# Optimization experiments

Hardware: AMD Instinct MI355X
Metric: run time of the kernel (lower is better)

## Reference

```python
import jax, jax.numpy as jnp
import numpy as np

B, L, D, H = 2, 2048, 1024, 16
HD = D // H
NEG = -1000000000.0


def setup_inputs() -> dict:
    key = jax.random.key(0)
    ks = jax.random.split(key, 11)
    s = 1.0 / np.sqrt(D)
    return {
        "q": jax.random.normal(ks[0], (B, L, D), jnp.float32),
        "k": jax.random.normal(ks[1], (B, L, D), jnp.float32),
        "v": jax.random.normal(ks[2], (B, L, D), jnp.float32),
        "mask": jnp.ones((B, L, L), jnp.int32),
        "Wq": jax.random.normal(ks[3], (D, D), jnp.float32) * s,
        "bq": jnp.zeros((D,), jnp.float32),
        "Wk": jax.random.normal(ks[4], (D, D), jnp.float32) * s,
        "bk": jnp.zeros((D,), jnp.float32),
        "Wv": jax.random.normal(ks[5], (D, D), jnp.float32) * s,
        "bv": jnp.zeros((D,), jnp.float32),
        "Wo": jax.random.normal(ks[6], (D, D), jnp.float32) * s,
        "bo": jnp.zeros((D,), jnp.float32),
    }


def _split(x):
    # [B,L,D] -> [B,H,L,HD]
    return x.reshape(B, L, H, HD).transpose(0, 2, 1, 3)


def reference(q, k, v, mask, Wq, bq, Wk, bk, Wv, bv, Wo, bo):
    Q = _split(q @ Wq.T + bq)
    K = _split(k @ Wk.T + bk)
    V = _split(v @ Wv.T + bv)
    scores = jnp.einsum("bhqd,bhkd->bhqk", Q, K) / jnp.sqrt(jnp.float32(HD))
    m = mask[:, None, :, :]  # [B,1,L,L]
    scores = jnp.where(m == 0, NEG, scores)
    attn = jax.nn.softmax(scores, axis=-1)
    out = jnp.einsum("bhqk,bhkd->bhqd", attn, V)
    out = out.transpose(0, 2, 1, 3).reshape(B, L, D)
    out = out @ Wo.T + bo
    return out, attn
```

## Files before the change

### kernel.cpp

```cpp
#include <hip/hip_runtime.h>
#include <stdint.h>

#define BSZ 2
#define LSEQ 2048
#define DMOD 1024
#define NH 16
#define HDSZ 64
#define NT (LSEQ / 128)

typedef __attribute__((ext_vector_type(8))) short short8;
typedef __attribute__((ext_vector_type(4))) float f32x4;
typedef __attribute__((ext_vector_type(4))) unsigned short u16x4;
typedef __attribute__((ext_vector_type(4))) int i32x4;

#define MFMA16(a, b, c) __builtin_amdgcn_mfma_f32_16x16x32_bf16((a), (b), (c), 0, 0, 0)
#define EXP2F(x) __builtin_amdgcn_exp2f(x)

__device__ __forceinline__ unsigned short f2bf(float f) {
  union { float f; unsigned u; } x; x.f = f;
  unsigned u = x.u + 0x7fffu + ((x.u >> 16) & 1u);
  return (unsigned short)(u >> 16);
}

__device__ __forceinline__ unsigned cvt_pk_bf16(float lo, float hi) {
  unsigned r;
  asm("v_cvt_pk_bf16_f32 %0, %1, %2" : "=v"(r) : "v"(lo), "v"(hi));
  return r;
}

__device__ __forceinline__ short8 pack8_pk(f32x4 lo, f32x4 hi) {
  union { short8 s; unsigned u[4]; } r;
  r.u[0] = cvt_pk_bf16(lo[0], lo[1]);
  r.u[1] = cvt_pk_bf16(lo[2], lo[3]);
  r.u[2] = cvt_pk_bf16(hi[0], hi[1]);
  r.u[3] = cvt_pk_bf16(hi[2], hi[3]);
  return r.s;
}

__device__ __forceinline__ u16x4 pack4_pk(float a, float b, float c, float d) {
  union { u16x4 p; unsigned u[2]; } r;
  r.u[0] = cvt_pk_bf16(a, b);
  r.u[1] = cvt_pk_bf16(c, d);
  return r.p;
}

template <int AF32, int OUTF32>
__global__ __launch_bounds__(256) void gemm_bt(
    const void* __restrict__ A0, const void* __restrict__ A1, const void* __restrict__ A2,
    const float* __restrict__ W0, const float* __restrict__ W1, const float* __restrict__ W2,
    const float* __restrict__ b0, const float* __restrict__ b1, const float* __restrict__ b2,
    void* __restrict__ C0, void* __restrict__ C1, void* __restrict__ C2,
    float s0, float s1, float s2, int vtz, int M, int N, int K,
    const int* __restrict__ mask, int* __restrict__ flags) {
  const int z = blockIdx.z;
  const int tid = threadIdx.x;
  __shared__ int red[4];

  if (z == 3) {
    const int t0 = (blockIdx.x + 32 * blockIdx.y) * 2;
#pragma unroll
    for (int t = t0; t < t0 + 2; ++t) {
      const int b_ = t >> 8, qt = (t >> 4) & 15, ktt = t & 15;
      const int r = tid >> 1, c = (tid & 1) * 64;
      const int* mr = mask + (size_t)b_ * LSEQ * LSEQ + (size_t)(qt * 128 + r) * LSEQ +
                      ktt * 128 + c;
      int ok = 1;
#pragma unroll
      for (int j = 0; j < 16; j++) {
        i32x4 v = __builtin_nontemporal_load((const i32x4*)(mr + j * 4));
        ok &= (v[0] != 0) & (v[1] != 0) & (v[2] != 0) & (v[3] != 0);
      }
      unsigned long long vote = __ballot(ok);
      if ((tid & 63) == 0) red[tid >> 6] = (vote == ~0ull) ? 1 : 0;
      __syncthreads();
      if (tid == 0) flags[(b_ * 16 + qt) * 16 + ktt] = red[0] & red[1] & red[2] & red[3];
      __syncthreads();
    }
    return;
  }

  const void* A = (z == 0) ? A0 : ((z == 1) ? A1 : A2);
  const float* W = (z == 0) ? W0 : ((z == 1) ? W1 : W2);
  const float* bias = (z == 0) ? b0 : ((z == 1) ? b1 : b2);
  void* Cout = (z == 0) ? C0 : ((z == 1) ? C1 : C2);
  const float scale = (z == 0) ? s0 : ((z == 1) ? s1 : s2);

  __shared__ unsigned short As[128 * 40];
  __shared__ unsigned short Bs[128 * 40];

  const int lane = tid & 63;
  const int wid = tid >> 6;
  const int bm = blockIdx.x, bn = blockIdx.y;
  const int wm = (wid >> 1) * 64, wn = (wid & 1) * 64;

  f32x4 acc[4][4];
#pragma unroll
  for (int i = 0; i < 4; i++)
#pragma unroll
    for (int j = 0; j < 4; j++) acc[i][j] = (f32x4){0.f, 0.f, 0.f, 0.f};

  const int r0 = tid >> 2;
  const int c0 = (tid & 3) * 8;
  const float* Wg = W + (size_t)(bn * 128 + r0) * K + c0;

  f32x4 vaf[2][2], vbf[2][2];
  short8 vah[2];
  if constexpr (AF32) {
    const float* Ag = (const float*)A + (size_t)(bm * 128 + r0) * K + c0;
#pragma unroll
    for (int j = 0; j < 2; j++) {
      vaf[j][0] = *(const f32x4*)(Ag + (size_t)(j * 64) * K);
      vaf[j][1] = *(const f32x4*)(Ag + (size_t)(j * 64) * K + 4);
    }
  } else {
    const unsigned short* Ag = (const unsigned short*)A + (size_t)(bm * 128 + r0) * K + c0;
#pragma unroll
    for (int j = 0; j < 2; j++) vah[j] = *(const short8*)(Ag + (size_t)(j * 64) * K);
  }
#pragma unroll
  for (int j = 0; j < 2; j++) {
    vbf[j][0] = *(const f32x4*)(Wg + (size_t)(j * 64) * K);
    vbf[j][1] = *(const f32x4*)(Wg + (size_t)(j * 64) * K + 4);
  }

  for (int k0 = 0; k0 < K; k0 += 32) {
#pragma unroll
    for (int j = 0; j < 2; j++) {
      if constexpr (AF32)
        *(short8*)&As[(j * 64 + r0) * 40 + c0] = pack8_pk(vaf[j][0], vaf[j][1]);
      else
        *(short8*)&As[(j * 64 + r0) * 40 + c0] = vah[j];
      *(short8*)&Bs[(j * 64 + r0) * 40 + c0] = pack8_pk(vbf[j][0], vbf[j][1]);
    }
    __syncthreads();
    if (k0 + 32 < K) {
      if constexpr (AF32) {
        const float* Ag = (const float*)A + (size_t)(bm * 128 + r0) * K + c0 + k0 + 32;
#pragma unroll
        for (int j = 0; j < 2; j++) {
          vaf[j][0] = *(const f32x4*)(Ag + (size_t)(j * 64) * K);
          vaf[j][1] = *(const f32x4*)(Ag + (size_t)(j * 64) * K + 4);
        }
      } else {
        const unsigned short* Ag =
            (const unsigned short*)A + (size_t)(bm * 128 + r0) * K + c0 + k0 + 32;
#pragma unroll
        for (int j = 0; j < 2; j++) vah[j] = *(const short8*)(Ag + (size_t)(j * 64) * K);
      }
#pragma unroll
      for (int j = 0; j < 2; j++) {
        vbf[j][0] = *(const f32x4*)(Wg + (size_t)(j * 64) * K + k0 + 32);
        vbf[j][1] = *(const f32x4*)(Wg + (size_t)(j * 64) * K + k0 + 36);
      }
    }
    short8 af[4], bf[4];
#pragma unroll
    for (int i = 0; i < 4; i++)
      af[i] = *(const short8*)&As[(wm + i * 16 + (lane & 15)) * 40 + (lane >> 4) * 8];
#pragma unroll
    for (int i = 0; i < 4; i++)
      bf[i] = *(const short8*)&Bs[(wn + i * 16 + (lane & 15)) * 40 + (lane >> 4) * 8];
#pragma unroll
    for (int i = 0; i < 4; i++)
#pragma unroll
      for (int j = 0; j < 4; j++) acc[i][j] = MFMA16(af[i], bf[j], acc[i][j]);
    __syncthreads();
  }

  const bool vtrans = (z == vtz);
  const int crow = bm * 128 + wm + ((lane >> 4) & 3) * 4;
#pragma unroll
  for (int j = 0; j < 4; j++) {
    const int col = bn * 128 + wn + j * 16 + (lane & 15);
    const float bv = bias[col];
#pragma unroll
    for (int i = 0; i < 4; i++) {
      if (OUTF32) {
#pragma unroll
        for (int r = 0; r < 4; r++) {
          float vvv = (acc[i][j][r] + bv) * scale;
          ((float*)Cout)[(size_t)(crow + i * 16 + r) * N + col] = vvv;
        }
      } else if (vtrans) {
        u16x4 pk = pack4_pk((acc[i][j][0] + bv) * scale, (acc[i][j][1] + bv) * scale,
                            (acc[i][j][2] + bv) * scale, (acc[i][j][3] + bv) * scale);
        const int row = crow + i * 16;
        unsigned short* dst = (unsigned short*)Cout +
                              (size_t)(row >> 11) * DMOD * LSEQ + (size_t)col * LSEQ +
                              (row & (LSEQ - 1));
        *(u16x4*)dst = pk;
      } else {
#pragma unroll
        for (int r = 0; r < 4; r++) {
          float vvv = (acc[i][j][r] + bv) * scale;
          ((unsigned short*)Cout)[(size_t)(crow + i * 16 + r) * N + col] =
              (unsigned short)(cvt_pk_bf16(vvv, vvv) & 0xffffu);
        }
      }
    }
  }
}

__global__ __launch_bounds__(256) void attn_kernel(
    const unsigned short* __restrict__ Qp, const unsigned short* __restrict__ Kp,
    const unsigned short* __restrict__ Vt, const int* __restrict__ mask,
    const int* __restrict__ flags, float* __restrict__ attn_out,
    unsigned short* __restrict__ ctx) {
  __shared__ unsigned short Ks[128 * 64];
  __shared__ unsigned short Ps[4][32][136];

  const int tid = threadIdx.x, lane = tid & 63, wid = tid >> 6;
  const int l15 = lane & 15, lg = lane >> 4;

  const int wgid = blockIdx.x + gridDim.x * blockIdx.y;
  const int jj = wgid >> 3;
  const int bh = (wgid & 7) * 4 + (jj >> 4);
  const int qt = jj & 15;
  const int q0 = qt * 128;
  const int b = bh >> 4, h = bh & 15;

  const unsigned short* Qh = Qp + (size_t)b * LSEQ * DMOD + h * HDSZ;
  const unsigned short* Kh = Kp + (size_t)b * LSEQ * DMOD + h * HDSZ;
  const unsigned short* Vh = Vt + (size_t)b * DMOD * LSEQ + (size_t)h * HDSZ * LSEQ;
  const int* mb = mask + (size_t)b * LSEQ * LSEQ;
  const int* frow = flags + (b * 16 + qt) * 16;
  float* ah = attn_out + (size_t)bh * LSEQ * LSEQ;

  const int wq0 = q0 + wid * 32;

  short8 qf[2][2];
#pragma unroll
  for (int fq = 0; fq < 2; fq++)
#pragma unroll
    for (int ks = 0; ks < 2; ks++)
      qf[fq][ks] = *(const short8*)(Qh + (size_t)(wq0 + fq * 16 + l15) * DMOD +
                                    ks * 32 + lg * 8);

  const int sr = tid >> 1;
  const unsigned short* Kst = Kh + (size_t)sr * DMOD + (tid & 1) * 32;
  const int swz_w = (sr & 7) << 4;

  float den[2] = {0.f, 0.f};
  short8 ka[4];
#pragma unroll
  for (int j = 0; j < 4; j++) ka[j] = *(const short8*)(Kst + j * 8);

  for (int kt = 0; kt < NT; ++kt) {
    __syncthreads();
#pragma unroll
    for (int j = 0; j < 4; j++)
      *(short8*)&Ks[sr * 64 + (((((tid & 1) * 64) + j * 16) ^ swz_w) >> 1)] = ka[j];
    __syncthreads();
    if (kt + 1 < NT) {
#pragma unroll
      for (int j = 0; j < 4; j++)
        ka[j] = *(const short8*)(Kst + (size_t)(kt + 1) * 128 * DMOD + j * 8);
    }
    const bool fast = frow[kt] != 0;
    if (fast) {
#pragma unroll
      for (int fn = 0; fn < 8; fn++) {
        const int krow = fn * 16 + l15;
        const int rb = krow * 64, rx = (krow & 7) << 4;
        short8 kf0 = *(const short8*)&Ks[rb + (((lg * 16) ^ rx) >> 1)];
        short8 kf1 = *(const short8*)&Ks[rb + (((64 + lg * 16) ^ rx) >> 1)];
#pragma unroll
        for (int fq = 0; fq < 2; fq++) {
          f32x4 s = (f32x4){0.f, 0.f, 0.f, 0.f};
          s = MFMA16(kf0, qf[fq][0], s);
          s = MFMA16(kf1, qf[fq][1], s);
          den[fq] += EXP2F(s[0]) + EXP2F(s[1]) + EXP2F(s[2]) + EXP2F(s[3]);
        }
      }
    } else {
      const int k0 = kt * 128;
#pragma unroll
      for (int fn = 0; fn < 8; fn++) {
        const int krow = fn * 16 + l15;
        const int rb = krow * 64, rx = (krow & 7) << 4;
        short8 kf0 = *(const short8*)&Ks[rb + (((lg * 16) ^ rx) >> 1)];
        short8 kf1 = *(const short8*)&Ks[rb + (((64 + lg * 16) ^ rx) >> 1)];
#pragma unroll
        for (int fq = 0; fq < 2; fq++) {
          const int qrow = wq0 + fq * 16 + l15;
          f32x4 s = (f32x4){0.f, 0.f, 0.f, 0.f};
          s = MFMA16(kf0, qf[fq][0], s);
          s = MFMA16(kf1, qf[fq][1], s);
          i32x4 m4 = *(const i32x4*)(mb + (size_t)qrow * LSEQ + k0 + fn * 16 + lg * 4);
          den[fq] += (m4[0] != 0) ? EXP2F(s[0]) : 0.f;
          den[fq] += (m4[1] != 0) ? EXP2F(s[1]) : 0.f;
          den[fq] += (m4[2] != 0) ? EXP2F(s[2]) : 0.f;
          den[fq] += (m4[3] != 0) ? EXP2F(s[3]) : 0.f;
        }
      }
    }
  }
  float inv[2];
#pragma unroll
  for (int fq = 0; fq < 2; fq++) {
    den[fq] += __shfl_xor(den[fq], 16);
    den[fq] += __shfl_xor(den[fq], 32);
    inv[fq] = 1.0f / den[fq];
  }

  f32x4 oacc[2][4];
#pragma unroll
  for (int fq = 0; fq < 2; fq++)
#pragma unroll
    for (int fd = 0; fd < 4; fd++) oacc[fq][fd] = (f32x4){0.f, 0.f, 0.f, 0.f};

#pragma unroll
  for (int j = 0; j < 4; j++) ka[j] = *(const short8*)(Kst + j * 8);

  const unsigned short* Vbase = Vh + (size_t)l15 * LSEQ + lg * 8;

  for (int kt = 0; kt < NT; ++kt) {
    const int k0 = kt * 128;
    __syncthreads();
#pragma unroll
    for (int j = 0; j < 4; j++)
      *(short8*)&Ks[sr * 64 + (((((tid & 1) * 64) + j * 16) ^ swz_w) >> 1)] = ka[j];
    __syncthreads();
    if (kt + 1 < NT) {
#pragma unroll
      for (int j = 0; j < 4; j++)
        ka[j] = *(const short8*)(Kst + (size_t)(kt + 1) * 128 * DMOD + j * 8);
    }
    short8 vf[4][4];
#pragma unroll
    for (int fd = 0; fd < 4; fd++)
#pragma unroll
      for (int ks = 0; ks < 4; ks++)
        vf[fd][ks] = *(const short8*)(Vbase + (size_t)(fd * 16) * LSEQ + k0 + ks * 32);

    const bool fast = frow[kt] != 0;
    if (fast) {
#pragma unroll
      for (int fn = 0; fn < 8; fn++) {
        const int krow = fn * 16 + l15;
        const int rb = krow * 64, rx = (krow & 7) << 4;
        short8 kf0 = *(const short8*)&Ks[rb + (((lg * 16) ^ rx) >> 1)];
        short8 kf1 = *(const short8*)&Ks[rb + (((64 + lg * 16) ^ rx) >> 1)];
#pragma unroll
        for (int fq = 0; fq < 2; fq++) {
          f32x4 s = (f32x4){0.f, 0.f, 0.f, 0.f};
          s = MFMA16(kf0, qf[fq][0], s);
          s = MFMA16(kf1, qf[fq][1], s);
          f32x4 a;
          a[0] = EXP2F(s[0]) * inv[fq];
          a[1] = EXP2F(s[1]) * inv[fq];
          a[2] = EXP2F(s[2]) * inv[fq];
          a[3] = EXP2F(s[3]) * inv[fq];
          union { u16x4 pk; unsigned u[2]; } P;
          P.u[0] = cvt_pk_bf16(a[0], a[1]);
          P.u[1] = cvt_pk_bf16(a[2], a[3]);
          *(u16x4*)&Ps[wid][fq * 16 + l15][fn * 16 + lg * 4] = P.pk;
        }
      }
    } else {
#pragma unroll
      for (int fn = 0; fn < 8; fn++) {
        const int krow = fn * 16 + l15;
        const int rb = krow * 64, rx = (krow & 7) << 4;
        short8 kf0 = *(const short8*)&Ks[rb + (((lg * 16) ^ rx) >> 1)];
        short8 kf1 = *(const short8*)&Ks[rb + (((64 + lg * 16) ^ rx) >> 1)];
#pragma unroll
        for (int fq = 0; fq < 2; fq++) {
          const int qrow = wq0 + fq * 16 + l15;
          f32x4 s = (f32x4){0.f, 0.f, 0.f, 0.f};
          s = MFMA16(kf0, qf[fq][0], s);
          s = MFMA16(kf1, qf[fq][1], s);
          i32x4 m4 = *(const i32x4*)(mb + (size_t)qrow * LSEQ + k0 + fn * 16 + lg * 4);
          f32x4 a;
          a[0] = (m4[0] != 0) ? EXP2F(s[0]) * inv[fq] : 0.f;
          a[1] = (m4[1] != 0) ? EXP2F(s[1]) * inv[fq] : 0.f;
          a[2] = (m4[2] != 0) ? EXP2F(s[2]) * inv[fq] : 0.f;
          a[3] = (m4[3] != 0) ? EXP2F(s[3]) * inv[fq] : 0.f;
          union { u16x4 pk; unsigned u[2]; } P;
          P.u[0] = cvt_pk_bf16(a[0], a[1]);
          P.u[1] = cvt_pk_bf16(a[2], a[3]);
          *(u16x4*)&Ps[wid][fq * 16 + l15][fn * 16 + lg * 4] = P.pk;
        }
      }
    }
    short8 pa2[2][4];
#pragma unroll
    for (int fq = 0; fq < 2; fq++)
#pragma unroll
      for (int ks = 0; ks < 4; ks++)
        pa2[fq][ks] = *(const short8*)&Ps[wid][fq * 16 + l15][ks * 32 + lg * 8];
#pragma unroll
    for (int fd = 0; fd < 4; fd++)
#pragma unroll
      for (int fq = 0; fq < 2; fq++)
#pragma unroll
        for (int ks = 0; ks < 4; ks++)
          oacc[fq][fd] = MFMA16(pa2[fq][ks], vf[fd][ks], oacc[fq][fd]);

    {
      float* abase = ah + (size_t)wq0 * LSEQ + k0;
      const int rsel = lane >> 5, csel = (lane & 31) * 4;
#pragma unroll
      for (int i = 0; i < 16; i++) {
        const int qoff = i * 2 + rsel;
        unsigned long long d = *(const unsigned long long*)&Ps[wid][qoff][csel];
        unsigned d0 = (unsigned)d, d1 = (unsigned)(d >> 32);
        union { unsigned u; float f; } t0, t1, t2, t3;
        t0.u = d0 << 16;
        t1.u = d0 & 0xffff0000u;
        t2.u = d1 << 16;
        t3.u = d1 & 0xffff0000u;
        f32x4 a = (f32x4){t0.f, t1.f, t2.f, t3.f};
        __builtin_nontemporal_store(a, (f32x4*)(abase + (size_t)qoff * LSEQ + csel));
      }
    }
  }

  unsigned short* ch = ctx + (size_t)b * LSEQ * DMOD + h * HDSZ;
#pragma unroll
  for (int fq = 0; fq < 2; fq++)
#pragma unroll
    for (int fd = 0; fd < 4; fd++) {
      u16x4 pk = pack4_pk(oacc[fq][fd][0], oacc[fq][fd][1], oacc[fq][fd][2],
                          oacc[fq][fd][3]);
#pragma unroll
      for (int r = 0; r < 4; r++) {
        const int qr = wq0 + fq * 16 + lg * 4 + r;
        ch[(size_t)qr * DMOD + fd * 16 + l15] = pk[r];
      }
    }
}

extern "C" void kernel_launch(void* const* d_in, const int* in_sizes, int n_in,
                              void* d_out, int out_size, void* d_ws, size_t ws_size,
                              hipStream_t stream) {
  const float* q = (const float*)d_in[0];
  const float* k = (const float*)d_in[1];
  const float* v = (const float*)d_in[2];
  const int* mask = (const int*)d_in[3];
  const float* Wq = (const float*)d_in[4];
  const float* bq = (const float*)d_in[5];
  const float* Wk = (const float*)d_in[6];
  const float* bk = (const float*)d_in[7];
  const float* Wv = (const float*)d_in[8];
  const float* bv = (const float*)d_in[9];
  const float* Wo = (const float*)d_in[10];
  const float* bo = (const float*)d_in[11];

  float* out = (float*)d_out;
  float* attn = out + (size_t)BSZ * LSEQ * DMOD;

  const size_t NQKV = (size_t)BSZ * LSEQ * DMOD;

  int* flags = (int*)out;

  unsigned short* Qp = (unsigned short*)d_ws;
  unsigned short* Kp = Qp + NQKV;
  unsigned short* Vt = Kp + NQKV;
  unsigned short* ctx = Vt + NQKV;

  gemm_bt<1, 0><<<dim3(32, 8, 4), 256, 0, stream>>>(
      q, k, v, Wq, Wk, Wv, bq, bk, bv, (void*)Qp, (void*)Kp, (void*)Vt,
      0.18033688011112042f, 1.0f, 1.0f, 2, BSZ * LSEQ, DMOD, DMOD, mask, flags);

  attn_kernel<<<dim3(LSEQ / 128, BSZ * NH), 256, 0, stream>>>(Qp, Kp, Vt, mask, flags,
                                                              attn, ctx);

  gemm_bt<0, 1><<<dim3(32, 8, 1), 256, 0, stream>>>(
      ctx, ctx, ctx, Wo, Wo, Wo, bo, bo, bo, (void*)out, (void*)out, (void*)out,
      1.0f, 1.0f, 1.0f, -1, BSZ * LSEQ, DMOD, DMOD, nullptr, nullptr);
}
```

Before: 229.3 us.

## Halve attention query tile to 64 rows per block, doubling grid size

Each attention workgroup now handles 64 query rows (16 per wave) instead of 128, so the grid grows from 512 to 1024 blocks and per-thread register use drops (single Q fragment, 4 output accumulators, smaller P buffer in LDS). V fragments are loaded per output column group just before use instead of all up front. This aims to raise occupancy and spread the bandwidth-heavy attention-probability writes over more CUs, at the cost of each K tile being loaded and QK^T recomputed by twice as many blocks.

```diff
diff --git a/kernel.cpp b/kernel.cpp
--- a/kernel.cpp
+++ b/kernel.cpp
@@ -207,40 +207,38 @@
     const int* __restrict__ flags, float* __restrict__ attn_out,
     unsigned short* __restrict__ ctx) {
   __shared__ unsigned short Ks[128 * 64];
-  __shared__ unsigned short Ps[4][32][136];
+  __shared__ unsigned short Ps[4][16][136];
 
   const int tid = threadIdx.x, lane = tid & 63, wid = tid >> 6;
   const int l15 = lane & 15, lg = lane >> 4;
 
   const int wgid = blockIdx.x + gridDim.x * blockIdx.y;
   const int jj = wgid >> 3;
-  const int bh = (wgid & 7) * 4 + (jj >> 4);
-  const int qt = jj & 15;
-  const int q0 = qt * 128;
+  const int bh = (wgid & 7) * 4 + (jj >> 5);
+  const int qt = jj & 31;
+  const int q0 = qt * 64;
   const int b = bh >> 4, h = bh & 15;
 
   const unsigned short* Qh = Qp + (size_t)b * LSEQ * DMOD + h * HDSZ;
   const unsigned short* Kh = Kp + (size_t)b * LSEQ * DMOD + h * HDSZ;
   const unsigned short* Vh = Vt + (size_t)b * DMOD * LSEQ + (size_t)h * HDSZ * LSEQ;
   const int* mb = mask + (size_t)b * LSEQ * LSEQ;
-  const int* frow = flags + (b * 16 + qt) * 16;
+  const int* frow = flags + (b * 16 + (q0 >> 7)) * 16;
   float* ah = attn_out + (size_t)bh * LSEQ * LSEQ;
 
-  const int wq0 = q0 + wid * 32;
-
-  short8 qf[2][2];
-#pragma unroll
-  for (int fq = 0; fq < 2; fq++)
-#pragma unroll
-    for (int ks = 0; ks < 2; ks++)
-      qf[fq][ks] = *(const short8*)(Qh + (size_t)(wq0 + fq * 16 + l15) * DMOD +
-                                    ks * 32 + lg * 8);
+  const int wq0 = q0 + wid * 16;
+  const int qrow = wq0 + l15;
+
+  short8 qf[2];
+#pragma unroll
+  for (int ks = 0; ks < 2; ks++)
+    qf[ks] = *(const short8*)(Qh + (size_t)qrow * DMOD + ks * 32 + lg * 8);
 
   const int sr = tid >> 1;
   const unsigned short* Kst = Kh + (size_t)sr * DMOD + (tid & 1) * 32;
   const int swz_w = (sr & 7) << 4;
 
-  float den[2] = {0.f, 0.f};
+  float den = 0.f;
   short8 ka[4];
 #pragma unroll
   for (int j = 0; j < 4; j++) ka[j] = *(const short8*)(Kst + j * 8);
@@ -264,13 +262,10 @@
         const int rb = krow * 64, rx = (krow & 7) << 4;
         short8 kf0 = *(const short8*)&Ks[rb + (((lg * 16) ^ rx) >> 1)];
         short8 kf1 = *(const short8*)&Ks[rb + (((64 + lg * 16) ^ rx) >> 1)];
-#pragma unroll
-        for (int fq = 0; fq < 2; fq++) {
-          f32x4 s = (f32x4){0.f, 0.f, 0.f, 0.f};
-          s = MFMA16(kf0, qf[fq][0], s);
-          s = MFMA16(kf1, qf[fq][1], s);
-          den[fq] += EXP2F(s[0]) + EXP2F(s[1]) + EXP2F(s[2]) + EXP2F(s[3]);
-        }
+        f32x4 s = (f32x4){0.f, 0.f, 0.f, 0.f};
+        s = MFMA16(kf0, qf[0], s);
+        s = MFMA16(kf1, qf[1], s);
+        den += EXP2F(s[0]) + EXP2F(s[1]) + EXP2F(s[2]) + EXP2F(s[3]);
       }
     } else {
       const int k0 = kt * 128;
@@ -280,34 +275,24 @@
         const int rb = krow * 64, rx = (krow & 7) << 4;
         short8 kf0 = *(const short8*)&Ks[rb + (((lg * 16) ^ rx) >> 1)];
         short8 kf1 = *(const short8*)&Ks[rb + (((64 + lg * 16) ^ rx) >> 1)];
-#pragma unroll
-        for (int fq = 0; fq < 2; fq++) {
-          const int qrow = wq0 + fq * 16 + l15;
-          f32x4 s = (f32x4){0.f, 0.f, 0.f, 0.f};
-          s = MFMA16(kf0, qf[fq][0], s);
-          s = MFMA16(kf1, qf[fq][1], s);
-          i32x4 m4 = *(const i32x4*)(mb + (size_t)qrow * LSEQ + k0 + fn * 16 + lg * 4);
-          den[fq] += (m4[0] != 0) ? EXP2F(s[0]) : 0.f;
-          den[fq] += (m4[1] != 0) ? EXP2F(s[1]) : 0.f;
-          den[fq] += (m4[2] != 0) ? EXP2F(s[2]) : 0.f;
-          den[fq] += (m4[3] != 0) ? EXP2F(s[3]) : 0.f;
-        }
-      }
-    }
-  }
-  float inv[2];
-#pragma unroll
-  for (int fq = 0; fq < 2; fq++) {
-    den[fq] += __shfl_xor(den[fq], 16);
-    den[fq] += __shfl_xor(den[fq], 32);
-    inv[fq] = 1.0f / den[fq];
-  }
-
-  f32x4 oacc[2][4];
-#pragma unroll
-  for (int fq = 0; fq < 2; fq++)
-#pragma unroll
-    for (int fd = 0; fd < 4; fd++) oacc[fq][fd] = (f32x4){0.f, 0.f, 0.f, 0.f};
+        f32x4 s = (f32x4){0.f, 0.f, 0.f, 0.f};
+        s = MFMA16(kf0, qf[0], s);
+        s = MFMA16(kf1, qf[1], s);
+        i32x4 m4 = *(const i32x4*)(mb + (size_t)qrow * LSEQ + k0 + fn * 16 + lg * 4);
+        den += (m4[0] != 0) ? EXP2F(s[0]) : 0.f;
+        den += (m4[1] != 0) ? EXP2F(s[1]) : 0.f;
+        den += (m4[2] != 0) ? EXP2F(s[2]) : 0.f;
+        den += (m4[3] != 0) ? EXP2F(s[3]) : 0.f;
+      }
+    }
+  }
+  den += __shfl_xor(den, 16);
+  den += __shfl_xor(den, 32);
+  const float inv = 1.0f / den;
+
+  f32x4 oacc[4];
+#pragma unroll
+  for (int fd = 0; fd < 4; fd++) oacc[fd] = (f32x4){0.f, 0.f, 0.f, 0.f};
 
 #pragma unroll
   for (int j = 0; j < 4; j++) ka[j] = *(const short8*)(Kst + j * 8);
@@ -326,12 +311,6 @@
       for (int j = 0; j < 4; j++)
         ka[j] = *(const short8*)(Kst + (size_t)(kt + 1) * 128 * DMOD + j * 8);
     }
-    short8 vf[4][4];
-#pragma unroll
-    for (int fd = 0; fd < 4; fd++)
-#pragma unroll
-      for (int ks = 0; ks < 4; ks++)
-        vf[fd][ks] = *(const short8*)(Vbase + (size_t)(fd * 16) * LSEQ + k0 + ks * 32);
 
     const bool fast = frow[kt] != 0;
     if (fast) {
@@ -341,21 +320,18 @@
         const int rb = krow * 64, rx = (krow & 7) << 4;
         short8 kf0 = *(const short8*)&Ks[rb + (((lg * 16) ^ rx) >> 1)];
         short8 kf1 = *(const short8*)&Ks[rb + (((64 + lg * 16) ^ rx) >> 1)];
-#pragma unroll
-        for (int fq = 0; fq < 2; fq++) {
-          f32x4 s = (f32x4){0.f, 0.f, 0.f, 0.f};
-          s = MFMA16(kf0, qf[fq][0], s);
-          s = MFMA16(kf1, qf[fq][1], s);
-          f32x4 a;
-          a[0] = EXP2F(s[0]) * inv[fq];
-          a[1] = EXP2F(s[1]) * inv[fq];
-          a[2] = EXP2F(s[2]) * inv[fq];
-          a[3] = EXP2F(s[3]) * inv[fq];
-          union { u16x4 pk; unsigned u[2]; } P;
-          P.u[0] = cvt_pk_bf16(a[0], a[1]);
-          P.u[1] = cvt_pk_bf16(a[2], a[3]);
-          *(u16x4*)&Ps[wid][fq * 16 + l15][fn * 16 + lg * 4] = P.pk;
-        }
+        f32x4 s = (f32x4){0.f, 0.f, 0.f, 0.f};
+        s = MFMA16(kf0, qf[0], s);
+        s = MFMA16(kf1, qf[1], s);
+        f32x4 a;
+        a[0] = EXP2F(s[0]) * inv;
+        a[1] = EXP2F(s[1]) * inv;
+        a[2] = EXP2F(s[2]) * inv;
+        a[3] = EXP2F(s[3]) * inv;
+        union { u16x4 pk; unsigned u[2]; } P;
+        P.u[0] = cvt_pk_bf16(a[0], a[1]);
+        P.u[1] = cvt_pk_bf16(a[2], a[3]);
+        *(u16x4*)&Ps[wid][l15][fn * 16 + lg * 4] = P.pk;
       }
     } else {
 #pragma unroll
@@ -364,44 +340,40 @@
         const int rb = krow * 64, rx = (krow & 7) << 4;
         short8 kf0 = *(const short8*)&Ks[rb + (((lg * 16) ^ rx) >> 1)];
         short8 kf1 = *(const short8*)&Ks[rb + (((64 + lg * 16) ^ rx) >> 1)];
-#pragma unroll
-        for (int fq = 0; fq < 2; fq++) {
-          const int qrow = wq0 + fq * 16 + l15;
-          f32x4 s = (f32x4){0.f, 0.f, 0.f, 0.f};
-          s = MFMA16(kf0, qf[fq][0], s);
-          s = MFMA16(kf1, qf[fq][1], s);
-          i32x4 m4 = *(const i32x4*)(mb + (size_t)qrow * LSEQ + k0 + fn * 16 + lg * 4);
-          f32x4 a;
-          a[0] = (m4[0] != 0) ? EXP2F(s[0]) * inv[fq] : 0.f;
-          a[1] = (m4[1] != 0) ? EXP2F(s[1]) * inv[fq] : 0.f;
-          a[2] = (m4[2] != 0) ? EXP2F(s[2]) * inv[fq] : 0.f;
-          a[3] = (m4[3] != 0) ? EXP2F(s[3]) * inv[fq] : 0.f;
-          union { u16x4 pk; unsigned u[2]; } P;
-          P.u[0] = cvt_pk_bf16(a[0], a[1]);
-          P.u[1] = cvt_pk_bf16(a[2], a[3]);
-          *(u16x4*)&Ps[wid][fq * 16 + l15][fn * 16 + lg * 4] = P.pk;
-        }
-      }
-    }
-    short8 pa2[2][4];
-#pragma unroll
-    for (int fq = 0; fq < 2; fq++)
+        f32x4 s = (f32x4){0.f, 0.f, 0.f, 0.f};
+        s = MFMA16(kf0, qf[0], s);
+        s = MFMA16(kf1, qf[1], s);
+        i32x4 m4 = *(const i32x4*)(mb + (size_t)qrow * LSEQ + k0 + fn * 16 + lg * 4);
+        f32x4 a;
+        a[0] = (m4[0] != 0) ? EXP2F(s[0]) * inv : 0.f;
+        a[1] = (m4[1] != 0) ? EXP2F(s[1]) * inv : 0.f;
+        a[2] = (m4[2] != 0) ? EXP2F(s[2]) * inv : 0.f;
+        a[3] = (m4[3] != 0) ? EXP2F(s[3]) * inv : 0.f;
+        union { u16x4 pk; unsigned u[2]; } P;
+        P.u[0] = cvt_pk_bf16(a[0], a[1]);
+        P.u[1] = cvt_pk_bf16(a[2], a[3]);
+        *(u16x4*)&Ps[wid][l15][fn * 16 + lg * 4] = P.pk;
+      }
+    }
+    short8 pa2[4];
+#pragma unroll
+    for (int ks = 0; ks < 4; ks++)
+      pa2[ks] = *(const short8*)&Ps[wid][l15][ks * 32 + lg * 8];
+#pragma unroll
+    for (int fd = 0; fd < 4; fd++) {
+      short8 vfd[4];
 #pragma unroll
       for (int ks = 0; ks < 4; ks++)
-        pa2[fq][ks] = *(const short8*)&Ps[wid][fq * 16 + l15][ks * 32 + lg * 8];
-#pragma unroll
-    for (int fd = 0; fd < 4; fd++)
-#pragma unroll
-      for (int fq = 0; fq < 2; fq++)
-#pragma unroll
-        for (int ks = 0; ks < 4; ks++)
-          oacc[fq][fd] = MFMA16(pa2[fq][ks], vf[fd][ks], oacc[fq][fd]);
+        vfd[ks] = *(const short8*)(Vbase + (size_t)(fd * 16) * LSEQ + k0 + ks * 32);
+#pragma unroll
+      for (int ks = 0; ks < 4; ks++) oacc[fd] = MFMA16(pa2[ks], vfd[ks], oacc[fd]);
+    }
 
     {
       float* abase = ah + (size_t)wq0 * LSEQ + k0;
       const int rsel = lane >> 5, csel = (lane & 31) * 4;
 #pragma unroll
-      for (int i = 0; i < 16; i++) {
+      for (int i = 0; i < 8; i++) {
         const int qoff = i * 2 + rsel;
         unsigned long long d = *(const unsigned long long*)&Ps[wid][qoff][csel];
         unsigned d0 = (unsigned)d, d1 = (unsigned)(d >> 32);
@@ -418,17 +390,14 @@
 
   unsigned short* ch = ctx + (size_t)b * LSEQ * DMOD + h * HDSZ;
 #pragma unroll
-  for (int fq = 0; fq < 2; fq++)
-#pragma unroll
-    for (int fd = 0; fd < 4; fd++) {
-      u16x4 pk = pack4_pk(oacc[fq][fd][0], oacc[fq][fd][1], oacc[fq][fd][2],
-                          oacc[fq][fd][3]);
-#pragma unroll
-      for (int r = 0; r < 4; r++) {
-        const int qr = wq0 + fq * 16 + lg * 4 + r;
-        ch[(size_t)qr * DMOD + fd * 16 + l15] = pk[r];
-      }
-    }
+  for (int fd = 0; fd < 4; fd++) {
+    u16x4 pk = pack4_pk(oacc[fd][0], oacc[fd][1], oacc[fd][2], oacc[fd][3]);
+#pragma unroll
+    for (int r = 0; r < 4; r++) {
+      const int qr = wq0 + lg * 4 + r;
+      ch[(size_t)qr * DMOD + fd * 16 + l15] = pk[r];
+    }
+  }
 }
 
 extern "C" void kernel_launch(void* const* d_in, const int* in_sizes, int n_in,
@@ -463,8 +432,7 @@
       q, k, v, Wq, Wk, Wv, bq, bk, bv, (void*)Qp, (void*)Kp, (void*)Vt,
       0.18033688011112042f, 1.0f, 1.0f, 2, BSZ * LSEQ, DMOD, DMOD, mask, flags);
 
-  attn_kernel<<<dim3(LSEQ / 128, BSZ * NH), 256, 0, stream>>>(Qp, Kp, Vt, mask, flags,
-                                                              attn, ctx);
+  attn_kernel<<<dim3(32, 32), 256, 0, stream>>>(Qp, Kp, Vt, mask, flags, attn, ctx);
 
   gemm_bt<0, 1><<<dim3(32, 8, 1), 256, 0, stream>>>(
       ctx, ctx, ctx, Wo, Wo, Wo, bo, bo, bo, (void*)out, (void*)out, (void*)out,
```

Measured after the change: 259.5 us. +13.2%, slower.
